# Kernel tuning notes

Measured on AMD Instinct MI355X. Metric: run time of the kernel, lower is better.

Reference implementation:

```python
import jax, jax.numpy as jnp
import numpy as np

B, S, T = 8, 2048, 128  # batch, seq_len, token_embedding_dim (== dep_transformed_dim, required by source bug)


def setup_inputs() -> dict:
    key = jax.random.key(0)
    k1, k2, k3, k4, k5, k6, k7 = jax.random.split(key, 7)
    sT = 1.0 / np.sqrt(T)
    sS = 1.0 / np.sqrt(S)
    return {
        "token_embeddings": jax.random.normal(k1, (B, S, T), jnp.float32),
        "dep_embeddings": jax.random.normal(k2, (B, S, T), jnp.float32),  # dead input (source bug), kept for fidelity
        "dep_heads": jax.random.randint(k3, (B, S), 0, S, jnp.int32),
        # composition_transform = Bilinear(T, T, T): weight [T_out, T_in1, T_in2], bias [T_out]
        "W_comp": jax.random.uniform(k4, (T, T, T), jnp.float32, -sT, sT),
        "b_comp": jax.random.uniform(k5, (T,), jnp.float32, -sT, sT),
        # reduction_transform = Linear(S, 1)
        "w_red": jax.random.uniform(k6, (1, S), jnp.float32, -sS, sS),
        "b_red": jax.random.uniform(k7, (1,), jnp.float32, -sS, sS),
    }


def reference(token_embeddings, dep_embeddings, dep_heads, W_comp, b_comp, w_red, b_red):
    # Faithful to source semantics (including the bug where dep_transform output is
    # discarded and tanh is applied to token_embeddings instead):
    #   dense[b,i,j,:] = tanh( bilinear(token[b,j], mask(i==heads[b,j]) * tanh(token[b,j])) )
    #   out[b,i,t]     = sum_j w_red[j] * dense[b,i,j,t] + b_red
    # Where mask is zero, bilinear collapses to its bias, so we never materialize
    # the [B,S,S,T] tensor: compute the 'active' value per token j and scatter-add
    # the delta vs. the bias-only baseline into row i = dep_heads[b,j].
    h = jnp.tanh(token_embeddings)                                   # [B,S,T]
    val = jnp.einsum('bsp,tpq,bsq->bst', token_embeddings, W_comp, h) + b_comp  # [B,S,T]
    act = jnp.tanh(val)                                              # active (masked-in) values
    base_val = jnp.tanh(b_comp)                                      # [T] value where mask is zero
    w = w_red[0]                                                     # [S], reduction weights over j
    base = jnp.sum(w) * base_val + b_red[0]                          # [T] bias-only row
    delta = w[None, :, None] * (act - base_val)                      # [B,S,T]
    b_idx = jnp.arange(token_embeddings.shape[0])[:, None]           # [B,1]
    out = base + jnp.zeros_like(act).at[b_idx, dep_heads].add(delta) # scatter over head rows
    return out
```

## Files before the change

kernel.cpp:

```cpp
#include <hip/hip_runtime.h>
#include <hip/hip_fp16.h>
#include <math.h>

#define S_LEN 2048
#define T_DIM 128
#define BM 64
#define NBLK 256

typedef _Float16 half8 __attribute__((ext_vector_type(8)));
typedef float floatx16 __attribute__((ext_vector_type(16)));

__global__ __launch_bounds__(256) void convert_w_kernel(
    const float* __restrict__ W, _Float16* __restrict__ W16f) {
  const int p = blockIdx.x;
  const int tc = blockIdx.y;
  const int tid = threadIdx.x;
#pragma unroll
  for (int i = 0; i < 2; ++i) {
    const int idx8 = i * 256 + tid;
    const int kc = idx8 >> 6;
    const int l = idx8 & 63;
    const int t = tc * 32 + (l & 31);
    const int q = kc * 16 + (l >> 5) * 8;
    const float* src = W + (size_t)t * 16384 + (size_t)p * 128 + q;
    const float4 v0 = *(const float4*)(src);
    const float4 v1 = *(const float4*)(src + 4);
    half8 h;
    h[0] = (_Float16)v0.x; h[1] = (_Float16)v0.y;
    h[2] = (_Float16)v0.z; h[3] = (_Float16)v0.w;
    h[4] = (_Float16)v1.x; h[5] = (_Float16)v1.y;
    h[6] = (_Float16)v1.z; h[7] = (_Float16)v1.w;
    *(half8*)(W16f + (((size_t)p * 4 + tc) * 8 + kc) * 512 + l * 8) = h;
  }
}

__global__ __launch_bounds__(256) void init_out_kernel(
    const float* __restrict__ w_red, const float* __restrict__ b_comp,
    const float* __restrict__ b_red, float* __restrict__ out) {
  __shared__ float red[4];
  const int tid = threadIdx.x;
  float part = 0.f;
#pragma unroll
  for (int i = 0; i < 8; ++i) part += w_red[tid * 8 + i];
#pragma unroll
  for (int off = 32; off > 0; off >>= 1) part += __shfl_down(part, off, 64);
  if ((tid & 63) == 0) red[tid >> 6] = part;
  __syncthreads();
  const float Sw = red[0] + red[1] + red[2] + red[3];
  const float br = b_red[0];
  const size_t base = (size_t)blockIdx.x * 1024 + (size_t)tid * 4;
  const int t0 = (int)(base & 127);
  float4 v;
  v.x = Sw * tanhf(b_comp[t0 + 0]) + br;
  v.y = Sw * tanhf(b_comp[t0 + 1]) + br;
  v.z = Sw * tanhf(b_comp[t0 + 2]) + br;
  v.w = Sw * tanhf(b_comp[t0 + 3]) + br;
  *(float4*)(out + base) = v;
}

__global__ __launch_bounds__(512, 2) void main_kernel(
    const float* __restrict__ tok, const int* __restrict__ heads,
    const _Float16* __restrict__ W16f, const float* __restrict__ b_comp,
    const float* __restrict__ w_red, float* __restrict__ out) {
  __shared__ _Float16 tokT[128][64];
  __shared__ float red[2][64][128];

  const int tid = threadIdx.x;
  const int lane = tid & 63;
  const int wave = tid >> 6;
  const int th = wave & 1;
  const int kh = wave >> 1;
  const int l31 = lane & 31;
  const int lh = lane >> 5;
  const int blk = blockIdx.x;
  const size_t tokbase = (size_t)blk * BM * T_DIM;

#pragma unroll
  for (int i = 0; i < 4; ++i) {
    const int f4 = i * 512 + tid;
    const int m = f4 >> 5;
    const int p0 = (f4 & 31) << 2;
    const float4 v = *(const float4*)(tok + tokbase + (size_t)m * 128 + p0);
    tokT[p0 + 0][m] = (_Float16)v.x;
    tokT[p0 + 1][m] = (_Float16)v.y;
    tokT[p0 + 2][m] = (_Float16)v.z;
    tokT[p0 + 3][m] = (_Float16)v.w;
  }

  half8 h16[2][2];
#pragma unroll
  for (int mh = 0; mh < 2; ++mh) {
    const int m = mh * 32 + l31;
#pragma unroll
    for (int ks = 0; ks < 2; ++ks) {
      const int q0 = kh * 32 + ks * 16 + lh * 8;
      const float4 v0 = *(const float4*)(tok + tokbase + (size_t)m * 128 + q0);
      const float4 v1 = *(const float4*)(tok + tokbase + (size_t)m * 128 + q0 + 4);
      h16[mh][ks][0] = (_Float16)tanhf(v0.x);
      h16[mh][ks][1] = (_Float16)tanhf(v0.y);
      h16[mh][ks][2] = (_Float16)tanhf(v0.z);
      h16[mh][ks][3] = (_Float16)tanhf(v0.w);
      h16[mh][ks][4] = (_Float16)tanhf(v1.x);
      h16[mh][ks][5] = (_Float16)tanhf(v1.y);
      h16[mh][ks][6] = (_Float16)tanhf(v1.z);
      h16[mh][ks][7] = (_Float16)tanhf(v1.w);
    }
  }
  __syncthreads();

  int off[2][2];
#pragma unroll
  for (int tt = 0; tt < 2; ++tt)
#pragma unroll
    for (int ks = 0; ks < 2; ++ks)
      off[tt][ks] = (((th * 2 + tt) * 8 + kh * 2 + ks) << 9) + lane * 8;

  floatx16 acc[2][2];
#pragma unroll
  for (int mh = 0; mh < 2; ++mh)
#pragma unroll
    for (int tt = 0; tt < 2; ++tt)
#pragma unroll
      for (int r = 0; r < 16; ++r) acc[mh][tt][r] = 0.f;

  half8 bf0[2][2], bf1[2][2];

  auto loadB = [&](half8 (&bf)[2][2], int p) {
    const _Float16* wp = W16f + (size_t)p * 16384;
#pragma unroll
    for (int tt = 0; tt < 2; ++tt)
#pragma unroll
      for (int ks = 0; ks < 2; ++ks)
        bf[tt][ks] = *(const half8*)(wp + off[tt][ks]);
  };

  auto compute = [&](half8 (&bf)[2][2], int p) {
    const _Float16 tokh0 = tokT[p][l31];
    const _Float16 tokh1 = tokT[p][32 + l31];
    half8 a0k0 = h16[0][0] * tokh0;
    half8 a0k1 = h16[0][1] * tokh0;
    half8 a1k0 = h16[1][0] * tokh1;
    half8 a1k1 = h16[1][1] * tokh1;
    acc[0][0] = __builtin_amdgcn_mfma_f32_32x32x16_f16(a0k0, bf[0][0], acc[0][0], 0, 0, 0);
    acc[0][1] = __builtin_amdgcn_mfma_f32_32x32x16_f16(a0k0, bf[1][0], acc[0][1], 0, 0, 0);
    acc[1][0] = __builtin_amdgcn_mfma_f32_32x32x16_f16(a1k0, bf[0][0], acc[1][0], 0, 0, 0);
    acc[1][1] = __builtin_amdgcn_mfma_f32_32x32x16_f16(a1k0, bf[1][0], acc[1][1], 0, 0, 0);
    acc[0][0] = __builtin_amdgcn_mfma_f32_32x32x16_f16(a0k1, bf[0][1], acc[0][0], 0, 0, 0);
    acc[0][1] = __builtin_amdgcn_mfma_f32_32x32x16_f16(a0k1, bf[1][1], acc[0][1], 0, 0, 0);
    acc[1][0] = __builtin_amdgcn_mfma_f32_32x32x16_f16(a1k1, bf[0][1], acc[1][0], 0, 0, 0);
    acc[1][1] = __builtin_amdgcn_mfma_f32_32x32x16_f16(a1k1, bf[1][1], acc[1][1], 0, 0, 0);
  };

  loadB(bf0, 0);
  for (int p = 0; p < 128; p += 2) {
    loadB(bf1, p + 1);
    compute(bf0, p);
    if (p + 2 < 128) loadB(bf0, p + 2);
    compute(bf1, p + 1);
  }

  __syncthreads();
  float* R = &red[kh >> 1][0][0];
  if ((kh & 1) == 0) {
#pragma unroll
    for (int mh = 0; mh < 2; ++mh)
#pragma unroll
      for (int tt = 0; tt < 2; ++tt) {
        const int t = (th * 2 + tt) * 32 + l31;
#pragma unroll
        for (int r = 0; r < 16; ++r) {
          const int m = mh * 32 + (r & 3) + 8 * (r >> 2) + 4 * lh;
          R[m * 128 + t] = acc[mh][tt][r];
        }
      }
  }
  __syncthreads();
  if ((kh & 1) == 1) {
#pragma unroll
    for (int mh = 0; mh < 2; ++mh)
#pragma unroll
      for (int tt = 0; tt < 2; ++tt) {
        const int t = (th * 2 + tt) * 32 + l31;
#pragma unroll
        for (int r = 0; r < 16; ++r) {
          const int m = mh * 32 + (r & 3) + 8 * (r >> 2) + 4 * lh;
          R[m * 128 + t] += acc[mh][tt][r];
        }
      }
  }
  __syncthreads();

  const int t = tid & 127;
  const float bc = b_comp[t];
  const float tbc = tanhf(bc);
#pragma unroll
  for (int it = 0; it < 16; ++it) {
    const int m = it * 4 + (tid >> 7);
    const float v = red[0][m][t] + red[1][m][t];
    const int gm = blk * BM + m;
    const int b = gm >> 11;
    const int s = gm & 2047;
    const int head = heads[gm];
    const float wr = w_red[s];
    atomicAdd(out + ((size_t)b * S_LEN + head) * T_DIM + t,
              wr * (tanhf(v + bc) - tbc));
  }
}

extern "C" void kernel_launch(void* const* d_in, const int* in_sizes, int n_in,
                              void* d_out, int out_size, void* d_ws, size_t ws_size,
                              hipStream_t stream) {
  const float* tok    = (const float*)d_in[0];
  const int*   heads  = (const int*)d_in[2];
  const float* W      = (const float*)d_in[3];
  const float* b_comp = (const float*)d_in[4];
  const float* w_red  = (const float*)d_in[5];
  const float* b_red  = (const float*)d_in[6];
  float* out = (float*)d_out;
  _Float16* W16f = (_Float16*)d_ws;

  convert_w_kernel<<<dim3(128, 4), 256, 0, stream>>>(W, W16f);
  init_out_kernel<<<2048, 256, 0, stream>>>(w_red, b_comp, b_red, out);
  main_kernel<<<NBLK, 512, 0, stream>>>(tok, heads, W16f, b_comp, w_red, out);
}
```

Measured before the change: 169.2 us.

## Split bilinear p-dimension across blocks with larger M tile and separate epilogue

Each main-kernel block now handles 128 rows but only half of the p reduction range, so every loaded W fragment feeds twice as many MFMAs. The two half-sums are written as fp16 partials to workspace, and a new epilogue kernel adds them, applies tanh and bias, and scatters into the output with atomics. The W conversion kernel is reorganised to read W row-contiguously. In exchange the change adds an extra launch, a round-trip of partials through global memory, and extra fp16 rounding of the partial sums.

```diff
diff --git a/kernel.cpp b/kernel.cpp
--- a/kernel.cpp
+++ b/kernel.cpp
@@ -4,49 +4,54 @@
 
 #define S_LEN 2048
 #define T_DIM 128
-#define BM 64
+#define BM 128
 #define NBLK 256
+#define P_ELEMS (16384u * 128u)
+#define RSTRIDE 132
 
 typedef _Float16 half8 __attribute__((ext_vector_type(8)));
+typedef _Float16 half4 __attribute__((ext_vector_type(4)));
 typedef float floatx16 __attribute__((ext_vector_type(16)));
 
 __global__ __launch_bounds__(256) void convert_w_kernel(
     const float* __restrict__ W, _Float16* __restrict__ W16f) {
-  const int p = blockIdx.x;
-  const int tc = blockIdx.y;
+  const int t = blockIdx.x >> 1;
+  const int qh = blockIdx.x & 1;
   const int tid = threadIdx.x;
-#pragma unroll
-  for (int i = 0; i < 2; ++i) {
-    const int idx8 = i * 256 + tid;
-    const int kc = idx8 >> 6;
-    const int l = idx8 & 63;
-    const int t = tc * 32 + (l & 31);
-    const int q = kc * 16 + (l >> 5) * 8;
+  const int tc = t >> 5;
+  const int tl = t & 31;
+#pragma unroll
+  for (int it = 0; it < 4; ++it) {
+    const int e8 = it * 256 + tid;
+    const int p = e8 >> 3;
+    const int q = qh * 64 + (e8 & 7) * 8;
     const float* src = W + (size_t)t * 16384 + (size_t)p * 128 + q;
-    const float4 v0 = *(const float4*)(src);
+    const float4 v0 = *(const float4*)src;
     const float4 v1 = *(const float4*)(src + 4);
     half8 h;
     h[0] = (_Float16)v0.x; h[1] = (_Float16)v0.y;
     h[2] = (_Float16)v0.z; h[3] = (_Float16)v0.w;
     h[4] = (_Float16)v1.x; h[5] = (_Float16)v1.y;
     h[6] = (_Float16)v1.z; h[7] = (_Float16)v1.w;
-    *(half8*)(W16f + (((size_t)p * 4 + tc) * 8 + kc) * 512 + l * 8) = h;
+    const int kc = q >> 4;
+    const int lh2 = (q >> 3) & 1;
+    *(half8*)(W16f + ((size_t)((p * 4 + tc) * 8 + kc)) * 512 + lh2 * 256 + tl * 8) = h;
   }
 }
 
 __global__ __launch_bounds__(256) void init_out_kernel(
     const float* __restrict__ w_red, const float* __restrict__ b_comp,
     const float* __restrict__ b_red, float* __restrict__ out) {
-  __shared__ float red[4];
+  __shared__ float red4[4];
   const int tid = threadIdx.x;
   float part = 0.f;
 #pragma unroll
   for (int i = 0; i < 8; ++i) part += w_red[tid * 8 + i];
 #pragma unroll
   for (int off = 32; off > 0; off >>= 1) part += __shfl_down(part, off, 64);
-  if ((tid & 63) == 0) red[tid >> 6] = part;
+  if ((tid & 63) == 0) red4[tid >> 6] = part;
   __syncthreads();
-  const float Sw = red[0] + red[1] + red[2] + red[3];
+  const float Sw = red4[0] + red4[1] + red4[2] + red4[3];
   const float br = b_red[0];
   const size_t base = (size_t)blockIdx.x * 1024 + (size_t)tid * 4;
   const int t0 = (int)(base & 127);
@@ -59,11 +64,10 @@
 }
 
 __global__ __launch_bounds__(512, 2) void main_kernel(
-    const float* __restrict__ tok, const int* __restrict__ heads,
-    const _Float16* __restrict__ W16f, const float* __restrict__ b_comp,
-    const float* __restrict__ w_red, float* __restrict__ out) {
-  __shared__ _Float16 tokT[128][64];
-  __shared__ float red[2][64][128];
+    const float* __restrict__ tok, const _Float16* __restrict__ W16f,
+    _Float16* __restrict__ P) {
+  __shared__ _Float16 tokT2[64 * 128];
+  __shared__ float red[128 * RSTRIDE];
 
   const int tid = threadIdx.x;
   const int lane = tid & 63;
@@ -73,23 +77,26 @@
   const int l31 = lane & 31;
   const int lh = lane >> 5;
   const int blk = blockIdx.x;
-  const size_t tokbase = (size_t)blk * BM * T_DIM;
-
-#pragma unroll
-  for (int i = 0; i < 4; ++i) {
-    const int f4 = i * 512 + tid;
-    const int m = f4 >> 5;
-    const int p0 = (f4 & 31) << 2;
-    const float4 v = *(const float4*)(tok + tokbase + (size_t)m * 128 + p0);
-    tokT[p0 + 0][m] = (_Float16)v.x;
-    tokT[p0 + 1][m] = (_Float16)v.y;
-    tokT[p0 + 2][m] = (_Float16)v.z;
-    tokT[p0 + 3][m] = (_Float16)v.w;
-  }
-
-  half8 h16[2][2];
-#pragma unroll
-  for (int mh = 0; mh < 2; ++mh) {
+  const int ph = blk & 1;
+  const int mb = blk >> 1;
+  const size_t tokbase = (size_t)mb * BM * T_DIM;
+
+#pragma unroll
+  for (int it = 0; it < 4; ++it) {
+    const int f = it * 512 + tid;
+    const int m = f >> 4;
+    const int p0 = (f & 15) * 4;
+    const float4 v = *(const float4*)(tok + tokbase + (size_t)m * 128 + ph * 64 + p0);
+    const int mi = (m & 31) * 4 + (m >> 5);
+    tokT2[(p0 + 0) * 128 + mi] = (_Float16)v.x;
+    tokT2[(p0 + 1) * 128 + mi] = (_Float16)v.y;
+    tokT2[(p0 + 2) * 128 + mi] = (_Float16)v.z;
+    tokT2[(p0 + 3) * 128 + mi] = (_Float16)v.w;
+  }
+
+  half8 h16[4][2];
+#pragma unroll
+  for (int mh = 0; mh < 4; ++mh) {
     const int m = mh * 32 + l31;
 #pragma unroll
     for (int ks = 0; ks < 2; ++ks) {
@@ -115,18 +122,19 @@
     for (int ks = 0; ks < 2; ++ks)
       off[tt][ks] = (((th * 2 + tt) * 8 + kh * 2 + ks) << 9) + lane * 8;
 
-  floatx16 acc[2][2];
-#pragma unroll
-  for (int mh = 0; mh < 2; ++mh)
+  floatx16 acc[4][2];
+#pragma unroll
+  for (int mh = 0; mh < 4; ++mh)
 #pragma unroll
     for (int tt = 0; tt < 2; ++tt)
 #pragma unroll
       for (int r = 0; r < 16; ++r) acc[mh][tt][r] = 0.f;
 
   half8 bf0[2][2], bf1[2][2];
+  const _Float16* Wbase = W16f + (size_t)ph * 64 * 16384;
 
   auto loadB = [&](half8 (&bf)[2][2], int p) {
-    const _Float16* wp = W16f + (size_t)p * 16384;
+    const _Float16* wp = Wbase + (size_t)p * 16384;
 #pragma unroll
     for (int tt = 0; tt < 2; ++tt)
 #pragma unroll
@@ -135,75 +143,85 @@
   };
 
   auto compute = [&](half8 (&bf)[2][2], int p) {
-    const _Float16 tokh0 = tokT[p][l31];
-    const _Float16 tokh1 = tokT[p][32 + l31];
-    half8 a0k0 = h16[0][0] * tokh0;
-    half8 a0k1 = h16[0][1] * tokh0;
-    half8 a1k0 = h16[1][0] * tokh1;
-    half8 a1k1 = h16[1][1] * tokh1;
-    acc[0][0] = __builtin_amdgcn_mfma_f32_32x32x16_f16(a0k0, bf[0][0], acc[0][0], 0, 0, 0);
-    acc[0][1] = __builtin_amdgcn_mfma_f32_32x32x16_f16(a0k0, bf[1][0], acc[0][1], 0, 0, 0);
-    acc[1][0] = __builtin_amdgcn_mfma_f32_32x32x16_f16(a1k0, bf[0][0], acc[1][0], 0, 0, 0);
-    acc[1][1] = __builtin_amdgcn_mfma_f32_32x32x16_f16(a1k0, bf[1][0], acc[1][1], 0, 0, 0);
-    acc[0][0] = __builtin_amdgcn_mfma_f32_32x32x16_f16(a0k1, bf[0][1], acc[0][0], 0, 0, 0);
-    acc[0][1] = __builtin_amdgcn_mfma_f32_32x32x16_f16(a0k1, bf[1][1], acc[0][1], 0, 0, 0);
-    acc[1][0] = __builtin_amdgcn_mfma_f32_32x32x16_f16(a1k1, bf[0][1], acc[1][0], 0, 0, 0);
-    acc[1][1] = __builtin_amdgcn_mfma_f32_32x32x16_f16(a1k1, bf[1][1], acc[1][1], 0, 0, 0);
+    const half4 tk = *(const half4*)(tokT2 + p * 128 + l31 * 4);
+#pragma unroll
+    for (int ks = 0; ks < 2; ++ks) {
+      half8 a0 = h16[0][ks] * tk[0];
+      half8 a1 = h16[1][ks] * tk[1];
+      half8 a2 = h16[2][ks] * tk[2];
+      half8 a3 = h16[3][ks] * tk[3];
+      acc[0][0] = __builtin_amdgcn_mfma_f32_32x32x16_f16(a0, bf[0][ks], acc[0][0], 0, 0, 0);
+      acc[0][1] = __builtin_amdgcn_mfma_f32_32x32x16_f16(a0, bf[1][ks], acc[0][1], 0, 0, 0);
+      acc[1][0] = __builtin_amdgcn_mfma_f32_32x32x16_f16(a1, bf[0][ks], acc[1][0], 0, 0, 0);
+      acc[1][1] = __builtin_amdgcn_mfma_f32_32x32x16_f16(a1, bf[1][ks], acc[1][1], 0, 0, 0);
+      acc[2][0] = __builtin_amdgcn_mfma_f32_32x32x16_f16(a2, bf[0][ks], acc[2][0], 0, 0, 0);
+      acc[2][1] = __builtin_amdgcn_mfma_f32_32x32x16_f16(a2, bf[1][ks], acc[2][1], 0, 0, 0);
+      acc[3][0] = __builtin_amdgcn_mfma_f32_32x32x16_f16(a3, bf[0][ks], acc[3][0], 0, 0, 0);
+      acc[3][1] = __builtin_amdgcn_mfma_f32_32x32x16_f16(a3, bf[1][ks], acc[3][1], 0, 0, 0);
+    }
   };
 
   loadB(bf0, 0);
-  for (int p = 0; p < 128; p += 2) {
+  for (int p = 0; p < 64; p += 2) {
     loadB(bf1, p + 1);
     compute(bf0, p);
-    if (p + 2 < 128) loadB(bf0, p + 2);
+    if (p + 2 < 64) loadB(bf0, p + 2);
     compute(bf1, p + 1);
   }
 
   __syncthreads();
-  float* R = &red[kh >> 1][0][0];
-  if ((kh & 1) == 0) {
-#pragma unroll
-    for (int mh = 0; mh < 2; ++mh)
-#pragma unroll
-      for (int tt = 0; tt < 2; ++tt) {
-        const int t = (th * 2 + tt) * 32 + l31;
-#pragma unroll
-        for (int r = 0; r < 16; ++r) {
-          const int m = mh * 32 + (r & 3) + 8 * (r >> 2) + 4 * lh;
-          R[m * 128 + t] = acc[mh][tt][r];
+#pragma unroll
+  for (int phase = 0; phase < 4; ++phase) {
+    if (kh == phase) {
+#pragma unroll
+      for (int mh = 0; mh < 4; ++mh)
+#pragma unroll
+        for (int tt = 0; tt < 2; ++tt) {
+          const int tcol = (th * 2 + tt) * 32 + l31;
+#pragma unroll
+          for (int r = 0; r < 16; ++r) {
+            const int m_loc = (r & 3) + 8 * (r >> 2) + 4 * lh;
+            const int addr = (mh * 32 + m_loc) * RSTRIDE + tcol;
+            if (phase == 0) red[addr] = acc[mh][tt][r];
+            else            red[addr] += acc[mh][tt][r];
+          }
         }
-      }
-  }
-  __syncthreads();
-  if ((kh & 1) == 1) {
-#pragma unroll
-    for (int mh = 0; mh < 2; ++mh)
-#pragma unroll
-      for (int tt = 0; tt < 2; ++tt) {
-        const int t = (th * 2 + tt) * 32 + l31;
-#pragma unroll
-        for (int r = 0; r < 16; ++r) {
-          const int m = mh * 32 + (r & 3) + 8 * (r >> 2) + 4 * lh;
-          R[m * 128 + t] += acc[mh][tt][r];
-        }
-      }
-  }
-  __syncthreads();
-
-  const int t = tid & 127;
-  const float bc = b_comp[t];
-  const float tbc = tanhf(bc);
-#pragma unroll
-  for (int it = 0; it < 16; ++it) {
-    const int m = it * 4 + (tid >> 7);
-    const float v = red[0][m][t] + red[1][m][t];
-    const int gm = blk * BM + m;
-    const int b = gm >> 11;
-    const int s = gm & 2047;
-    const int head = heads[gm];
-    const float wr = w_red[s];
-    atomicAdd(out + ((size_t)b * S_LEN + head) * T_DIM + t,
-              wr * (tanhf(v + bc) - tbc));
+    }
+    __syncthreads();
+  }
+
+  _Float16* Pp = P + (size_t)ph * P_ELEMS;
+#pragma unroll
+  for (int it = 0; it < 4; ++it) {
+    const int chunk = it * 512 + tid;
+    const int m = chunk >> 4;
+    const int t0 = (chunk & 15) * 8;
+    half8 h;
+#pragma unroll
+    for (int j = 0; j < 8; ++j) h[j] = (_Float16)red[m * RSTRIDE + t0 + j];
+    *(half8*)(Pp + (size_t)(mb * BM + m) * 128 + t0) = h;
+  }
+}
+
+__global__ __launch_bounds__(256) void epilogue_kernel(
+    const _Float16* __restrict__ P, const int* __restrict__ heads,
+    const float* __restrict__ b_comp, const float* __restrict__ w_red,
+    float* __restrict__ out) {
+  const int gid = blockIdx.x * 256 + threadIdx.x;
+  const int m = gid >> 4;
+  const int t0 = (gid & 15) * 8;
+  const half8 p0 = *(const half8*)(P + (size_t)m * 128 + t0);
+  const half8 p1 = *(const half8*)(P + P_ELEMS + (size_t)m * 128 + t0);
+  const int b = m >> 11;
+  const int s = m & 2047;
+  const int head = heads[m];
+  const float wr = w_red[s];
+  float* orow = out + ((size_t)b * S_LEN + head) * T_DIM;
+#pragma unroll
+  for (int j = 0; j < 8; ++j) {
+    const float bc = b_comp[t0 + j];
+    const float v = (float)p0[j] + (float)p1[j] + bc;
+    atomicAdd(orow + t0 + j, wr * (tanhf(v) - tanhf(bc)));
   }
 }
 
@@ -217,9 +235,12 @@
   const float* w_red  = (const float*)d_in[5];
   const float* b_red  = (const float*)d_in[6];
   float* out = (float*)d_out;
+
   _Float16* W16f = (_Float16*)d_ws;
-
-  convert_w_kernel<<<dim3(128, 4), 256, 0, stream>>>(W, W16f);
+  _Float16* P    = (_Float16*)d_ws + 2097152;
+
+  convert_w_kernel<<<256, 256, 0, stream>>>(W, W16f);
   init_out_kernel<<<2048, 256, 0, stream>>>(w_red, b_comp, b_red, out);
-  main_kernel<<<NBLK, 512, 0, stream>>>(tok, heads, W16f, b_comp, w_red, out);
-}
+  main_kernel<<<NBLK, 512, 0, stream>>>(tok, W16f, P);
+  epilogue_kernel<<<1024, 256, 0, stream>>>(P, heads, b_comp, w_red, out);
+}
```

Result: slower. 215.0 us (+27.1%).
